# Kernel optimization log

Hardware: AMD Instinct MI355X
Metric: run time of the kernel (lower is better)

The kernel has to match this reference:

```python
import jax, jax.numpy as jnp
import numpy as np

D = 512       # feature dim of X0 (Linear(512,...) in emb)
DQK = D // 8  # SAGAN-style reduced query/key dim
B = 256
S = 255       # structured features -> N = S + 1 tokens


def _lin(key, fan_in, fan_out):
    kw, kb = jax.random.split(key)
    s = 1.0 / np.sqrt(fan_in)
    W = jax.random.uniform(kw, (fan_in, fan_out), jnp.float32, -s, s)
    b = jax.random.uniform(kb, (fan_out,), jnp.float32, -s, s)
    return W, b


def setup_inputs() -> dict:
    key = jax.random.key(0)
    ks = jax.random.split(key, 9)
    X0 = jax.random.normal(ks[0], (B, D), jnp.float32)
    X_struc = jax.random.normal(ks[1], (B, S), jnp.float32)
    Wq, bq = _lin(ks[2], D, DQK)
    Wk, bk = _lin(ks[3], D, DQK)
    Wv, bv = _lin(ks[4], D, D)
    gamma = jnp.zeros((), jnp.float32) + 0.5  # nonzero so attention path contributes
    W1, b1 = _lin(ks[5], D, 1024)
    W2, b2 = _lin(ks[6], 1024, 512)
    W3, b3 = _lin(ks[7], 512, 128)
    return {"X0": X0, "X_struc": X_struc, "Wq": Wq, "bq": bq, "Wk": Wk, "bk": bk,
            "Wv": Wv, "bv": bv, "gamma": gamma, "W1": W1, "b1": b1,
            "W2": W2, "b2": b2, "W3": W3, "b3": b3}


def reference(X0, X_struc, Wq, bq, Wk, bk, Wv, bv, gamma, W1, b1, W2, b2, W3, b3):
    # Batched outer product replaces the per-sample torch.mm loop:
    # X1[b, s, d] = X_struc[b, s] * X0[b, d]
    X1 = X_struc[:, :, None] * X0[:, None, :]            # [B, S, D]
    X = jnp.concatenate([X0[:, None, :], X1], axis=1)    # [B, N, D], N = S+1
    # SAGAN-style self-attention (Self_Attention(out_planes=512))
    Q = X @ Wq + bq                                      # [B, N, DQK]
    K = X @ Wk + bk                                      # [B, N, DQK]
    V = X @ Wv + bv                                      # [B, N, D]
    A = jax.nn.softmax(jnp.einsum('bnc,bmc->bnm', Q, K), axis=-1)  # [B, N, N]
    Y = gamma * jnp.einsum('bnm,bmd->bnd', A, V) + X     # residual
    # emb MLP: 512 -> 1024 -> 512 -> 128, ReLU after each layer
    h = jax.nn.relu(Y @ W1 + b1)
    h = jax.nn.relu(h @ W2 + b2)
    out = jax.nn.relu(h @ W3 + b3)                       # [B, N, 128]
    return out
```

## Files before the change

kernel.cpp:

```cpp
#include <hip/hip_runtime.h>
#include <hip/hip_bf16.h>

typedef __attribute__((ext_vector_type(8))) short s16x8;
typedef __attribute__((ext_vector_type(16))) float f32x16;

__device__ __forceinline__ unsigned short f2bfu(float x) {
  __hip_bfloat16 b = __float2bfloat16(x);
  return *reinterpret_cast<unsigned short*>(&b);
}

__device__ __forceinline__ unsigned int cvtpk(float a, float b) {
  unsigned int r;
  asm("v_cvt_pk_bf16_f32 %0, %1, %2" : "=v"(r) : "v"(a), "v"(b));
  return r;
}

__global__ __launch_bounds__(256) void prep1_k(
    const float* __restrict__ W2, const float* __restrict__ W3,
    const float* __restrict__ W1,
    unsigned short* __restrict__ W2P, unsigned short* __restrict__ W3P,
    unsigned short* __restrict__ W1P,
    const float* __restrict__ X0, const float* __restrict__ Wv,
    const float* __restrict__ Wq, const float* __restrict__ Wk,
    float* __restrict__ V0ws, float* __restrict__ QKws) {
  __shared__ __align__(16) char smc[65664];
  const int tid = threadIdx.x;
  const int blk = blockIdx.x;

  if (blk < 64) {
    unsigned short* lt = (unsigned short*)smc;
    if (blk < 32) {
      const int kb = blk;
#pragma unroll
      for (int i = 0; i < 16; ++i) {
        const int e4 = i * 256 + tid;
        const int r = e4 >> 7, c4 = (e4 & 127) * 4;
        const float4 v = *(const float4*)(W2 + (size_t)(kb * 32 + r) * 512 + c4);
        lt[r * 514 + c4 + 0] = f2bfu(v.x);
        lt[r * 514 + c4 + 1] = f2bfu(v.y);
        lt[r * 514 + c4 + 2] = f2bfu(v.z);
        lt[r * 514 + c4 + 3] = f2bfu(v.w);
      }
      __syncthreads();
#pragma unroll
      for (int i = 0; i < 8; ++i) {
        const int c = i * 256 + tid;
        const int kgl = c >> 10, nb = (c >> 6) & 15, l = c & 63;
        const int col = nb * 32 + (l & 31);
        const int k0 = kgl * 16 + (l >> 5) * 8;
        s16x8 v;
#pragma unroll
        for (int j = 0; j < 8; ++j) v[j] = lt[(k0 + j) * 514 + col];
        *(s16x8*)(W2P + ((size_t)((kb * 2 + kgl) * 16 + nb) * 64 + l) * 8) = v;
      }
    } else if (blk < 48) {
      const int kb = blk - 32;
#pragma unroll
      for (int i = 0; i < 32; ++i) {
        const int e4 = i * 256 + tid;
        const int r = e4 >> 8, c4 = (e4 & 255) * 4;
        const float4 v = *(const float4*)(W1 + (size_t)(kb * 32 + r) * 1024 + c4);
        lt[r * 1026 + c4 + 0] = f2bfu(v.x);
        lt[r * 1026 + c4 + 1] = f2bfu(v.y);
        lt[r * 1026 + c4 + 2] = f2bfu(v.z);
        lt[r * 1026 + c4 + 3] = f2bfu(v.w);
      }
      __syncthreads();
#pragma unroll
      for (int i = 0; i < 16; ++i) {
        const int c = i * 256 + tid;
        const int kgl = c >> 11, nb = (c >> 6) & 31, l = c & 63;
        const int col = nb * 32 + (l & 31);
        const int k0 = kgl * 16 + (l >> 5) * 8;
        s16x8 v;
#pragma unroll
        for (int j = 0; j < 8; ++j) v[j] = lt[(k0 + j) * 1026 + col];
        *(s16x8*)(W1P + ((size_t)((kb * 2 + kgl) * 32 + nb) * 64 + l) * 8) = v;
      }
    } else {
      const int kb = blk - 48;
#pragma unroll
      for (int i = 0; i < 4; ++i) {
        const int e4 = i * 256 + tid;
        const int r = e4 >> 5, c4 = (e4 & 31) * 4;
        const float4 v = *(const float4*)(W3 + (size_t)(kb * 32 + r) * 128 + c4);
        lt[r * 130 + c4 + 0] = f2bfu(v.x);
        lt[r * 130 + c4 + 1] = f2bfu(v.y);
        lt[r * 130 + c4 + 2] = f2bfu(v.z);
        lt[r * 130 + c4 + 3] = f2bfu(v.w);
      }
      __syncthreads();
#pragma unroll
      for (int i = 0; i < 2; ++i) {
        const int c = i * 256 + tid;
        const int kgl = c >> 8, nb = (c >> 6) & 3, l = c & 63;
        const int col = nb * 32 + (l & 31);
        const int k0 = kgl * 16 + (l >> 5) * 8;
        s16x8 v;
#pragma unroll
        for (int j = 0; j < 8; ++j) v[j] = lt[(k0 + j) * 130 + col];
        *(s16x8*)(W3P + ((size_t)((kb * 2 + kgl) * 4 + nb) * 64 + l) * 8) = v;
      }
    }
    return;
  }
  float* As = (float*)smc;
  float* Bs = (float*)(smc + 2176);
  const int r = blk - 64;
  const int bn = r % 10, bm = r / 10;
  const int tx = tid & 15, ty = tid >> 4;
  float acc[2][4] = {};
  for (int k0 = 0; k0 < 512; k0 += 16) {
    if (tid < 128) {
      const int row = tid >> 2, kk = (tid & 3) * 4;
      const float4 v = *(const float4*)(X0 + (size_t)(bm * 32 + row) * 512 + k0 + kk);
      As[row * 17 + kk] = v.x; As[row * 17 + kk + 1] = v.y;
      As[row * 17 + kk + 2] = v.z; As[row * 17 + kk + 3] = v.w;
    }
    {
      const int k = tid >> 4, n4 = (tid & 15) * 4;
      float4 v;
      if (bn < 8)       v = *(const float4*)(Wv + (size_t)(k0 + k) * 512 + bn * 64 + n4);
      else if (bn == 8) v = *(const float4*)(Wq + (size_t)(k0 + k) * 64 + n4);
      else              v = *(const float4*)(Wk + (size_t)(k0 + k) * 64 + n4);
      Bs[k * 68 + n4] = v.x; Bs[k * 68 + n4 + 1] = v.y;
      Bs[k * 68 + n4 + 2] = v.z; Bs[k * 68 + n4 + 3] = v.w;
    }
    __syncthreads();
#pragma unroll
    for (int kk = 0; kk < 16; ++kk) {
      float a[2], bb[4];
#pragma unroll
      for (int i = 0; i < 2; ++i) a[i] = As[(ty * 2 + i) * 17 + kk];
#pragma unroll
      for (int j = 0; j < 4; ++j) bb[j] = Bs[kk * 68 + tx * 4 + j];
#pragma unroll
      for (int i = 0; i < 2; ++i)
#pragma unroll
        for (int j = 0; j < 4; ++j) acc[i][j] = fmaf(a[i], bb[j], acc[i][j]);
    }
    __syncthreads();
  }
#pragma unroll
  for (int i = 0; i < 2; ++i) {
    const int row = bm * 32 + ty * 2 + i;
#pragma unroll
    for (int j = 0; j < 4; ++j) {
      const int n = tx * 4 + j;
      if (bn < 8)       V0ws[(size_t)row * 512 + bn * 64 + n] = acc[i][j];
      else if (bn == 8) QKws[(size_t)row * 128 + n] = acc[i][j];
      else              QKws[(size_t)row * 128 + 64 + n] = acc[i][j];
    }
  }
}

__global__ __launch_bounds__(256) void prep2_k(
    const float* __restrict__ Xs, const float* __restrict__ QKws,
    const float* __restrict__ bq, float* __restrict__ Wws,
    const float* __restrict__ V0ws, const float* __restrict__ X0,
    const float* __restrict__ bv, const float* __restrict__ W1,
    const unsigned short* __restrict__ W1P,
    const float* __restrict__ gp, const float* __restrict__ b1,
    float* __restrict__ Pws, float* __restrict__ Rws, float* __restrict__ Cws) {
  const int tid = threadIdx.x;
  if (blockIdx.x < 256) {
    const int b = blockIdx.x, t = tid;
    __shared__ float sv[256];
    __shared__ float scal[4];
    sv[t] = (t == 0) ? 1.0f : Xs[b * 255 + t - 1];
    __syncthreads();
    if (t == 0) {
      float al = 0, g2 = 0;
      for (int j = 0; j < 64; ++j) {
        al = fmaf(QKws[b * 128 + j], QKws[b * 128 + 64 + j], al);
        g2 = fmaf(bq[j], QKws[b * 128 + 64 + j], g2);
      }
      float mx = sv[0], mn = sv[0];
      for (int m2 = 1; m2 < 256; ++m2) { mx = fmaxf(mx, sv[m2]); mn = fminf(mn, sv[m2]); }
      scal[0] = al; scal[1] = g2; scal[2] = mx; scal[3] = mn;
    }
    __syncthreads();
    const float c = fmaf(scal[0], sv[tid], scal[1]);
    const float M = (c >= 0.f) ? c * scal[2] : c * scal[3];
    float Z = 0, Wm = 0;
    for (int m2 = 0; m2 < 256; ++m2) {
      const float e = __expf(fmaf(c, sv[m2], -M));
      Z += e;
      Wm = fmaf(sv[m2], e, Wm);
    }
    Wws[b * 256 + tid] = Wm / Z;
    return;
  }
  if (blockIdx.x < 260) {
    const int col = (blockIdx.x - 256) * 256 + tid;
    float a = 0;
    for (int d = 0; d < 512; ++d) a = fmaf(bv[d], W1[(size_t)d * 1024 + col], a);
    Cws[col] = fmaf(gp[0], a, b1[col]);
    return;
  }
  const int r = blockIdx.x - 260;
  const int pr = r >> 6;
  const int rem = r & 63;
  const int mb = rem >> 4, nb = rem & 15;
  const float* srcA = pr ? X0 : V0ws;
  float* dst = pr ? Rws : Pws;
  const int lane = tid & 63, w = tid >> 6;
  const int la31 = lane & 31, hi = lane >> 5;
  const int rowbase = mb * 64 + (w >> 1) * 32;
  const int nbW = nb * 2 + (w & 1);
  const float* ar = srcA + (size_t)(rowbase + la31) * 512 + hi * 8;
  const unsigned short* pBW = W1P + ((size_t)nbW * 64 + lane) * 8;

  f32x16 acc;
#pragma unroll
  for (int i = 0; i < 16; ++i) acc[i] = 0.f;

  float4 fa[2][2];
  s16x8 bst[2];
  fa[0][0] = *(const float4*)(ar);
  fa[0][1] = *(const float4*)(ar + 4);
  bst[0] = *(const s16x8*)(pBW);
  pBW += 16384;

#pragma unroll 2
  for (int kg = 0; kg < 32; ++kg) {
    const int par = kg & 1;
    if (kg < 31) {
      fa[par ^ 1][0] = *(const float4*)(ar + (kg + 1) * 16);
      fa[par ^ 1][1] = *(const float4*)(ar + (kg + 1) * 16 + 4);
      bst[par ^ 1] = *(const s16x8*)(pBW);
      pBW += 16384;
    }
    union { s16x8 v; unsigned int u[4]; } t;
    const float4 a0 = fa[par][0], a1 = fa[par][1];
    t.u[0] = cvtpk(a0.x, a0.y);
    t.u[1] = cvtpk(a0.z, a0.w);
    t.u[2] = cvtpk(a1.x, a1.y);
    t.u[3] = cvtpk(a1.z, a1.w);
    acc = __builtin_amdgcn_mfma_f32_32x32x16_bf16(t.v, bst[par], acc, 0, 0, 0);
  }
#pragma unroll
  for (int reg = 0; reg < 16; ++reg) {
    const int rowl = (reg & 3) + 8 * (reg >> 2) + 4 * hi;
    dst[(size_t)(rowbase + rowl) * 1024 + nbW * 32 + la31] = acc[reg];
  }
}

__global__ __launch_bounds__(512, 4) void fused_k(
    const float* __restrict__ Xs, const float* __restrict__ gp,
    const unsigned short* __restrict__ W2P,
    const float* __restrict__ b2,
    const unsigned short* __restrict__ W3P,
    const float* __restrict__ b3,
    const float* __restrict__ Cws, const float* __restrict__ Wws,
    const float* __restrict__ Pws, const float* __restrict__ Rws,
    float* __restrict__ out)
{
  __shared__ __align__(16) unsigned char sm[65536];
  unsigned short* smU = (unsigned short*)sm;
  float* PRC = (float*)(sm + 16384);
  const int tid = threadIdx.x;
  const int lane = tid & 63, wid = tid >> 6;
  const int la31 = lane & 31, hi = lane >> 5;
  const int m0 = blockIdx.x * 64;
  const int b = blockIdx.x >> 2;
  const float g = gp[0];

  const int rg = lane;
  const int tokg = (m0 & 255) + rg;
  const float gw = g * Wws[b * 256 + tokg];
  const float sr = (tokg == 0) ? 1.0f : Xs[b * 255 + tokg - 1];

#pragma unroll
  for (int i = 0; i < 6; ++i) {
    const int idx = i * 512 + tid;
    float v;
    if (idx < 1024)      v = Pws[b * 1024 + idx];
    else if (idx < 2048) v = Rws[b * 1024 + (idx - 1024)];
    else                 v = Cws[idx - 2048];
    PRC[idx] = v;
  }

  auto gen = [&](int buf, int step) {
    const int kb = step * 64 + wid * 8;
    float e[8];
#pragma unroll
    for (int j = 0; j < 8; j += 4) {
      const float4 Pv = *(const float4*)(PRC + kb + j);
      const float4 Rv = *(const float4*)(PRC + 1024 + kb + j);
      const float4 Cv = *(const float4*)(PRC + 2048 + kb + j);
      e[j + 0] = fmaxf(fmaf(gw, Pv.x, fmaf(sr, Rv.x, Cv.x)), 0.f);
      e[j + 1] = fmaxf(fmaf(gw, Pv.y, fmaf(sr, Rv.y, Cv.y)), 0.f);
      e[j + 2] = fmaxf(fmaf(gw, Pv.z, fmaf(sr, Rv.z, Cv.z)), 0.f);
      e[j + 3] = fmaxf(fmaf(gw, Pv.w, fmaf(sr, Rv.w, Cv.w)), 0.f);
    }
    union { s16x8 v; unsigned int u[4]; } t0;
    t0.u[0] = cvtpk(e[0], e[1]);  t0.u[1] = cvtpk(e[2], e[3]);
    t0.u[2] = cvtpk(e[4], e[5]);  t0.u[3] = cvtpk(e[6], e[7]);
    *(s16x8*)(sm + buf * 8192 + (wid * 64 + rg) * 16) = t0.v;
  };

  f32x16 acc[2][2];
#pragma unroll
  for (int mf = 0; mf < 2; ++mf)
#pragma unroll
    for (int nf = 0; nf < 2; ++nf)
#pragma unroll
      for (int i = 0; i < 16; ++i) acc[mf][nf][i] = 0.f;

  const unsigned short* pB = W2P + ((size_t)(wid * 2) * 64 + lane) * 8;
  s16x8 bst[2][2];
#pragma unroll
  for (int nf = 0; nf < 2; ++nf)
    bst[0][nf] = *(const s16x8*)(pB + nf * 512);
  pB += 8192;

  __syncthreads();
  gen(0, 0);

  for (int step = 0; step < 16; ++step) {
    __syncthreads();
    if (step < 15) gen((step + 1) & 1, step + 1);
    const int abase = (step & 1) * 8192;
#pragma unroll
    for (int kgl = 0; kgl < 4; ++kgl) {
      const int par = kgl & 1;
#pragma unroll
      for (int nf = 0; nf < 2; ++nf)
        bst[par ^ 1][nf] = *(const s16x8*)(pB + nf * 512);
      pB += 8192;
      s16x8 af[2];
#pragma unroll
      for (int mf = 0; mf < 2; ++mf)
        af[mf] = *(const s16x8*)(sm + abase + ((kgl * 2 + hi) * 64 + mf * 32 + la31) * 16);
#pragma unroll
      for (int nf = 0; nf < 2; ++nf)
#pragma unroll
        for (int mf = 0; mf < 2; ++mf)
          acc[mf][nf] = __builtin_amdgcn_mfma_f32_32x32x16_bf16(af[mf], bst[par][nf], acc[mf][nf], 0, 0, 0);
    }
  }
  __syncthreads();

#pragma unroll
  for (int nf = 0; nf < 2; ++nf) {
    const int col = wid * 64 + nf * 32 + la31;
    const float bb = b2[col];
    const int sc = col >> 3, c7 = col & 7;
#pragma unroll
    for (int mf = 0; mf < 2; ++mf) {
#pragma unroll
      for (int reg = 0; reg < 16; ++reg) {
        const int row = mf * 32 + (reg & 3) + 8 * (reg >> 2) + 4 * hi;
        const int sp = (sc & 56) | ((sc ^ row) & 7);
        smU[row * 512 + sp * 8 + c7] = f2bfu(fmaxf(acc[mf][nf][reg] + bb, 0.f));
      }
    }
  }
  __syncthreads();

  const int wr = wid >> 2, wc = wid & 3;
  f32x16 acc2;
#pragma unroll
  for (int i = 0; i < 16; ++i) acc2[i] = 0.f;

  const unsigned short* pW = W3P + ((size_t)wc * 64 + lane) * 8;
  s16x8 wst[2];
  wst[0] = *(const s16x8*)(pW);
  pW += 2048;
#pragma unroll 2
  for (int kg = 0; kg < 32; ++kg) {
    const int par = kg & 1;
    wst[par ^ 1] = *(const s16x8*)(pW);
    pW += 2048;
    const int s = kg * 2 + hi;
    const int row = wr * 32 + la31;
    const int sp = (s & 56) | ((s ^ row) & 7);
    const s16x8 afh = *(const s16x8*)(&sm[row * 1024 + (sp << 4)]);
    acc2 = __builtin_amdgcn_mfma_f32_32x32x16_bf16(afh, wst[par], acc2, 0, 0, 0);
  }

  {
    const int cB = wc * 32 + la31;
    const float b3v = b3[cB];
#pragma unroll
    for (int reg = 0; reg < 16; ++reg) {
      const int row = m0 + wr * 32 + (reg & 3) + 8 * (reg >> 2) + 4 * hi;
      out[(size_t)row * 128 + cB] = fmaxf(acc2[reg] + b3v, 0.f);
    }
  }
}

extern "C" void kernel_launch(void* const* d_in, const int* in_sizes, int n_in,
                              void* d_out, int out_size, void* d_ws, size_t ws_size,
                              hipStream_t stream) {
  const float* X0 = (const float*)d_in[0];
  const float* Xs = (const float*)d_in[1];
  const float* Wq = (const float*)d_in[2];
  const float* bq = (const float*)d_in[3];
  const float* Wk = (const float*)d_in[4];
  const float* bk = (const float*)d_in[5];
  const float* Wv = (const float*)d_in[6];
  const float* bv = (const float*)d_in[7];
  const float* gp = (const float*)d_in[8];
  const float* W1 = (const float*)d_in[9];
  const float* b1 = (const float*)d_in[10];
  const float* W2 = (const float*)d_in[11];
  const float* b2 = (const float*)d_in[12];
  const float* W3 = (const float*)d_in[13];
  const float* b3 = (const float*)d_in[14];

  char* ws = (char*)d_ws;
  float* Cws = (float*)(ws);
  float* Wws = (float*)(ws + 4096);
  float* Pws = (float*)(ws + 266240);
  float* Rws = (float*)(ws + 1314816);
  unsigned short* W2P = (unsigned short*)(ws + 2363392);
  unsigned short* W3P = (unsigned short*)(ws + 3411968);
  float* V0ws = (float*)(ws + 3543040);
  float* QKws = (float*)(ws + 4067328);
  unsigned short* W1P = (unsigned short*)(ws + 4198400);
  float* out = (float*)d_out;

  hipLaunchKernelGGL(prep1_k, dim3(144), dim3(256), 0, stream,
                     W2, W3, W1, W2P, W3P, W1P, X0, Wv, Wq, Wk, V0ws, QKws);
  hipLaunchKernelGGL(prep2_k, dim3(388), dim3(256), 0, stream,
                     Xs, QKws, bq, Wws, V0ws, X0, bv, W1, W1P, gp, b1, Pws, Rws, Cws);
  hipLaunchKernelGGL(fused_k, dim3(1024), dim3(512), 0, stream,
                     Xs, gp, W2P, b2, W3P, b3, Cws, Wws, Pws, Rws, out);
}
```

Before: 133.3 us.

## Use per-row GEMV for X0 projections and double the fused-kernel K-step size

```diff
diff --git a/kernel.cpp b/kernel.cpp
--- a/kernel.cpp
+++ b/kernel.cpp
@@ -104,53 +104,34 @@
     }
     return;
   }
-  float* As = (float*)smc;
-  float* Bs = (float*)(smc + 2176);
-  const int r = blk - 64;
-  const int bn = r % 10, bm = r / 10;
-  const int tx = tid & 15, ty = tid >> 4;
-  float acc[2][4] = {};
-  for (int k0 = 0; k0 < 512; k0 += 16) {
-    if (tid < 128) {
-      const int row = tid >> 2, kk = (tid & 3) * 4;
-      const float4 v = *(const float4*)(X0 + (size_t)(bm * 32 + row) * 512 + k0 + kk);
-      As[row * 17 + kk] = v.x; As[row * 17 + kk + 1] = v.y;
-      As[row * 17 + kk + 2] = v.z; As[row * 17 + kk + 3] = v.w;
-    }
-    {
-      const int k = tid >> 4, n4 = (tid & 15) * 4;
-      float4 v;
-      if (bn < 8)       v = *(const float4*)(Wv + (size_t)(k0 + k) * 512 + bn * 64 + n4);
-      else if (bn == 8) v = *(const float4*)(Wq + (size_t)(k0 + k) * 64 + n4);
-      else              v = *(const float4*)(Wk + (size_t)(k0 + k) * 64 + n4);
-      Bs[k * 68 + n4] = v.x; Bs[k * 68 + n4 + 1] = v.y;
-      Bs[k * 68 + n4 + 2] = v.z; Bs[k * 68 + n4 + 3] = v.w;
-    }
-    __syncthreads();
-#pragma unroll
-    for (int kk = 0; kk < 16; ++kk) {
-      float a[2], bb[4];
-#pragma unroll
-      for (int i = 0; i < 2; ++i) a[i] = As[(ty * 2 + i) * 17 + kk];
-#pragma unroll
-      for (int j = 0; j < 4; ++j) bb[j] = Bs[kk * 68 + tx * 4 + j];
-#pragma unroll
-      for (int i = 0; i < 2; ++i)
-#pragma unroll
-        for (int j = 0; j < 4; ++j) acc[i][j] = fmaf(a[i], bb[j], acc[i][j]);
-    }
-    __syncthreads();
-  }
-#pragma unroll
-  for (int i = 0; i < 2; ++i) {
-    const int row = bm * 32 + ty * 2 + i;
-#pragma unroll
-    for (int j = 0; j < 4; ++j) {
-      const int n = tx * 4 + j;
-      if (bn < 8)       V0ws[(size_t)row * 512 + bn * 64 + n] = acc[i][j];
-      else if (bn == 8) QKws[(size_t)row * 128 + n] = acc[i][j];
-      else              QKws[(size_t)row * 128 + 64 + n] = acc[i][j];
-    }
+  float* x0f = (float*)smc;
+  const int row = blk - 64;
+  x0f[tid] = X0[(size_t)row * 512 + tid];
+  x0f[tid + 256] = X0[(size_t)row * 512 + 256 + tid];
+  __syncthreads();
+  {
+    float a0 = 0, a1 = 0, b0 = 0, b1 = 0;
+#pragma unroll 8
+    for (int k = 0; k < 512; k += 2) {
+      const float xv0 = x0f[k], xv1 = x0f[k + 1];
+      a0 = fmaf(xv0, Wv[(size_t)k * 512 + tid], a0);
+      b0 = fmaf(xv1, Wv[(size_t)(k + 1) * 512 + tid], b0);
+      a1 = fmaf(xv0, Wv[(size_t)k * 512 + tid + 256], a1);
+      b1 = fmaf(xv1, Wv[(size_t)(k + 1) * 512 + tid + 256], b1);
+    }
+    V0ws[(size_t)row * 512 + tid] = a0 + b0;
+    V0ws[(size_t)row * 512 + tid + 256] = a1 + b1;
+  }
+  if (tid < 128) {
+    const float* W = (tid < 64) ? Wq : Wk;
+    const int j = tid & 63;
+    float a = 0, bpart = 0;
+#pragma unroll 8
+    for (int k = 0; k < 512; k += 2) {
+      a = fmaf(x0f[k], W[(size_t)k * 64 + j], a);
+      bpart = fmaf(x0f[k + 1], W[(size_t)(k + 1) * 64 + j], bpart);
+    }
+    QKws[(size_t)row * 128 + tid] = a + bpart;
   }
 }
 
@@ -258,7 +239,7 @@
 {
   __shared__ __align__(16) unsigned char sm[65536];
   unsigned short* smU = (unsigned short*)sm;
-  float* PRC = (float*)(sm + 16384);
+  float* PRC = (float*)(sm + 32768);
   const int tid = threadIdx.x;
   const int lane = tid & 63, wid = tid >> 6;
   const int la31 = lane & 31, hi = lane >> 5;
@@ -282,22 +263,26 @@
   }
 
   auto gen = [&](int buf, int step) {
-    const int kb = step * 64 + wid * 8;
-    float e[8];
-#pragma unroll
-    for (int j = 0; j < 8; j += 4) {
-      const float4 Pv = *(const float4*)(PRC + kb + j);
-      const float4 Rv = *(const float4*)(PRC + 1024 + kb + j);
-      const float4 Cv = *(const float4*)(PRC + 2048 + kb + j);
-      e[j + 0] = fmaxf(fmaf(gw, Pv.x, fmaf(sr, Rv.x, Cv.x)), 0.f);
-      e[j + 1] = fmaxf(fmaf(gw, Pv.y, fmaf(sr, Rv.y, Cv.y)), 0.f);
-      e[j + 2] = fmaxf(fmaf(gw, Pv.z, fmaf(sr, Rv.z, Cv.z)), 0.f);
-      e[j + 3] = fmaxf(fmaf(gw, Pv.w, fmaf(sr, Rv.w, Cv.w)), 0.f);
-    }
-    union { s16x8 v; unsigned int u[4]; } t0;
-    t0.u[0] = cvtpk(e[0], e[1]);  t0.u[1] = cvtpk(e[2], e[3]);
-    t0.u[2] = cvtpk(e[4], e[5]);  t0.u[3] = cvtpk(e[6], e[7]);
-    *(s16x8*)(sm + buf * 8192 + (wid * 64 + rg) * 16) = t0.v;
+#pragma unroll
+    for (int gsub = 0; gsub < 2; ++gsub) {
+      const int s = gsub * 8 + wid;
+      const int kb = step * 128 + s * 8;
+      float e[8];
+#pragma unroll
+      for (int j = 0; j < 8; j += 4) {
+        const float4 Pv = *(const float4*)(PRC + kb + j);
+        const float4 Rv = *(const float4*)(PRC + 1024 + kb + j);
+        const float4 Cv = *(const float4*)(PRC + 2048 + kb + j);
+        e[j + 0] = fmaxf(fmaf(gw, Pv.x, fmaf(sr, Rv.x, Cv.x)), 0.f);
+        e[j + 1] = fmaxf(fmaf(gw, Pv.y, fmaf(sr, Rv.y, Cv.y)), 0.f);
+        e[j + 2] = fmaxf(fmaf(gw, Pv.z, fmaf(sr, Rv.z, Cv.z)), 0.f);
+        e[j + 3] = fmaxf(fmaf(gw, Pv.w, fmaf(sr, Rv.w, Cv.w)), 0.f);
+      }
+      union { s16x8 v; unsigned int u[4]; } t0;
+      t0.u[0] = cvtpk(e[0], e[1]);  t0.u[1] = cvtpk(e[2], e[3]);
+      t0.u[2] = cvtpk(e[4], e[5]);  t0.u[3] = cvtpk(e[6], e[7]);
+      *(s16x8*)(sm + buf * 16384 + (s * 64 + rg) * 16) = t0.v;
+    }
   };
 
   f32x16 acc[2][2];
@@ -318,12 +303,12 @@
   __syncthreads();
   gen(0, 0);
 
-  for (int step = 0; step < 16; ++step) {
+  for (int step = 0; step < 8; ++step) {
     __syncthreads();
-    if (step < 15) gen((step + 1) & 1, step + 1);
-    const int abase = (step & 1) * 8192;
-#pragma unroll
-    for (int kgl = 0; kgl < 4; ++kgl) {
+    if (step < 7) gen((step + 1) & 1, step + 1);
+    const int abase = (step & 1) * 16384;
+#pragma unroll
+    for (int kgl = 0; kgl < 8; ++kgl) {
       const int par = kgl & 1;
 #pragma unroll
       for (int nf = 0; nf < 2; ++nf)
@@ -422,7 +407,7 @@
   unsigned short* W1P = (unsigned short*)(ws + 4198400);
   float* out = (float*)d_out;
 
-  hipLaunchKernelGGL(prep1_k, dim3(144), dim3(256), 0, stream,
+  hipLaunchKernelGGL(prep1_k, dim3(320), dim3(256), 0, stream,
                      W2, W3, W1, W2P, W3P, W1P, X0, Wv, Wq, Wk, V0ws, QKws);
   hipLaunchKernelGGL(prep2_k, dim3(388), dim3(256), 0, stream,
                      Xs, QKws, bq, Wws, V0ws, X0, bv, W1, W1P, gp, b1, Pws, Rws, Cws);
```

Measured after the change: 126.3 us. 5.2% less time.
